# Optimization experiments

Measured on AMD Instinct MI355X. Metric: run time of the kernel, lower is better.

## Reference

```python
import jax, jax.numpy as jnp
import numpy as np

B, N, D_IN, D_OUT = 16, 2048, 128, 128

def setup_inputs() -> dict:
    key = jax.random.key(0)
    ks = jax.random.split(key, 8)
    x = jax.random.normal(ks[0], (B, N, D_IN), dtype=jnp.float32)
    adj = jax.random.randint(ks[1], (N, N), 0, 2).astype(jnp.float32)
    # Conv1d(kernel_size=1) weights, PyTorch default uniform init scale
    s_emb = 1.0 / np.sqrt(D_IN)
    W_emb = jax.random.uniform(ks[2], (D_OUT, D_IN), jnp.float32, -s_emb, s_emb)
    b_emb = jax.random.uniform(ks[3], (D_OUT,), jnp.float32, -s_emb, s_emb)
    s_qk = 1.0 / np.sqrt(D_OUT)
    w_q = jax.random.uniform(ks[4], (D_OUT,), jnp.float32, -s_qk, s_qk)
    b_q = jax.random.uniform(ks[5], (1,), jnp.float32, -s_qk, s_qk)
    w_k = jax.random.uniform(ks[6], (D_OUT,), jnp.float32, -s_qk, s_qk)
    b_k = jax.random.uniform(ks[7], (1,), jnp.float32, -s_qk, s_qk)
    return {"x": x, "adj": adj, "W_emb": W_emb, "b_emb": b_emb,
            "w_q": w_q, "b_q": b_q, "w_k": w_k, "b_k": b_k}

def reference(x, adj, W_emb, b_emb, w_q, b_q, w_k, b_k):
    # emb_conv: 1x1 conv over node dim == per-node linear  [B,N,D_out]
    seq_fts = jnp.einsum('bni,oi->bno', x, W_emb) + b_emb
    # q_conv / k_conv: project to scalar per node  [B,N]
    q = jnp.einsum('bnd,d->bn', seq_fts, w_q) + b_q  # f_1_t squeezed
    k = jnp.einsum('bnd,d->bn', seq_fts, w_k) + b_k  # f_2_t squeezed
    # f[b,i,j] = f_1_t[b,0,j] + f_2_t^T[b,i,0] = q[b,j] + k[b,i]
    f = k[:, :, None] + q[:, None, :]                 # [B,N,N]
    f = jax.nn.leaky_relu(adj[None, :, :] * f, negative_slope=0.01)
    coefs = jax.nn.softmax(f, axis=1)                 # softmax over dim=1 (rows)
    vals = jnp.einsum('bij,bjd->bid', coefs, seq_fts)  # [B,N,D_out]
    return vals
```

## Files before the change

kernel.cpp:

```cpp
#include <hip/hip_runtime.h>
#include <hip/hip_bf16.h>
#include <stdint.h>

#define B_ 16
#define N_ 2048
#define D_ 128

typedef __bf16 bf16_t;
typedef bf16_t bf16x8 __attribute__((ext_vector_type(8)));
typedef float f32x4 __attribute__((ext_vector_type(4)));

__global__ __launch_bounds__(256) void k_pack_adj(const float* __restrict__ adj,
                                                  unsigned int* __restrict__ bits) {
    int t = blockIdx.x * 256 + threadIdx.x;
    float v = adj[t];
    unsigned long long m = __ballot(v > 0.5f);
    if ((t & 63) == 0) {
        int i = t >> 11;
        int j = t & 2047;
        bits[i * 64 + (j >> 5)]     = (unsigned int)m;
        bits[i * 64 + (j >> 5) + 1] = (unsigned int)(m >> 32);
    }
}

__global__ __launch_bounds__(256, 1) void k_emb(const float* __restrict__ x,
                                                const float* __restrict__ W,
                                                const float* __restrict__ be,
                                                const float* __restrict__ wq,
                                                const float* __restrict__ wk,
                                                float* __restrict__ sfT,
                                                float* __restrict__ qa,
                                                float* __restrict__ ka) {
    __shared__ float xs[32][132];
    __shared__ float ws[32][132];
    __shared__ float qs[128], ks[128];
    int b  = blockIdx.y;
    int n0 = blockIdx.x * 128;
    int tid = threadIdx.x;
    int tx = tid & 15, ty = tid >> 4;
    if (tid < 128) { qs[tid] = 0.f; ks[tid] = 0.f; }

    float acc[8][8] = {};
    f32x4 xr[4], wr[4];

    auto loadregs = [&](int kc) {
#pragma unroll
        for (int s = 0; s < 4; ++s) {
            int p = tid + 256 * s;
            int n = p >> 3, kq = p & 7;
            xr[s] = *(const f32x4*)(x + ((size_t)(b * N_ + n0 + n)) * D_ + kc * 32 + kq * 4);
            wr[s] = *(const f32x4*)(W + (size_t)n * D_ + kc * 32 + kq * 4);
        }
    };
    auto writelds = [&]() {
#pragma unroll
        for (int s = 0; s < 4; ++s) {
            int p = tid + 256 * s;
            int n = p >> 3, kq = p & 7;
#pragma unroll
            for (int u = 0; u < 4; ++u) {
                xs[kq * 4 + u][n] = xr[s][u];
                ws[kq * 4 + u][n] = wr[s][u];
            }
        }
    };

    loadregs(0);
    for (int kc = 0; kc < 4; ++kc) {
        writelds();
        __syncthreads();
        if (kc < 3) loadregs(kc + 1);
        for (int k = 0; k < 32; ++k) {
            f32x4 xv0 = *(const f32x4*)&xs[k][tx * 8];
            f32x4 xv1 = *(const f32x4*)&xs[k][tx * 8 + 4];
            f32x4 wv0 = *(const f32x4*)&ws[k][ty * 8];
            f32x4 wv1 = *(const f32x4*)&ws[k][ty * 8 + 4];
#pragma unroll
            for (int i = 0; i < 8; ++i) {
                float xi = (i < 4) ? xv0[i] : xv1[i - 4];
#pragma unroll
                for (int j = 0; j < 8; ++j) {
                    float wj = (j < 4) ? wv0[j] : wv1[j - 4];
                    acc[i][j] += xi * wj;
                }
            }
        }
        __syncthreads();
    }

    float qp[8] = {}, kp[8] = {};
#pragma unroll
    for (int j = 0; j < 8; ++j) {
        int d = ty * 8 + j;
        float bj  = be[d];
        float wqj = wq[d];
        float wkj = wk[d];
        f32x4 o0, o1;
#pragma unroll
        for (int i = 0; i < 4; ++i) { o0[i] = acc[i][j] + bj; o1[i] = acc[4 + i][j] + bj; }
#pragma unroll
        for (int i = 0; i < 4; ++i) {
            qp[i]     += o0[i] * wqj;  kp[i]     += o0[i] * wkj;
            qp[4 + i] += o1[i] * wqj;  kp[4 + i] += o1[i] * wkj;
        }
        float* dst = sfT + ((size_t)b * D_ + d) * N_ + n0 + tx * 8;
        *(f32x4*)dst = o0;
        *(f32x4*)(dst + 4) = o1;
    }
#pragma unroll
    for (int i = 0; i < 8; ++i) {
        atomicAdd(&qs[tx * 8 + i], qp[i]);
        atomicAdd(&ks[tx * 8 + i], kp[i]);
    }
    __syncthreads();
    if (tid < 128) {
        qa[b * N_ + n0 + tid] = qs[tid];
        ka[b * N_ + n0 + tid] = ks[tid];
    }
}

__global__ __launch_bounds__(256) void k_exp(const float* __restrict__ bq,
                                             const float* __restrict__ bk,
                                             float* __restrict__ qa, float* __restrict__ ka,
                                             float* __restrict__ Eq, float* __restrict__ eqs,
                                             float* __restrict__ Ek, float* __restrict__ eks) {
    int t = blockIdx.x * 256 + threadIdx.x;
    float aq = qa[t] + bq[0];
    float ak = ka[t] + bk[0];
    qa[t] = aq;            ka[t] = ak;
    Eq[t] = expf(aq);      eqs[t] = expf(0.01f * aq);
    Ek[t] = expf(ak);      eks[t] = expf(0.01f * ak);
}

__global__ __launch_bounds__(256) void k_denom(const unsigned int* __restrict__ bits,
                                               const float* __restrict__ qa,
                                               const float* __restrict__ ka,
                                               const float* __restrict__ Eq,
                                               const float* __restrict__ eqs,
                                               const float* __restrict__ Ek,
                                               const float* __restrict__ eks,
                                               float* __restrict__ denom) {
    int jt  = blockIdx.x;
    int b   = blockIdx.y;
    int seg = blockIdx.z;
    int j = jt * 256 + threadIdx.x;
    float qj  = qa[b * N_ + j];
    float Eqj = Eq[b * N_ + j];
    float eqj = eqs[b * N_ + j];
    int shift = j & 31;
    int wid   = j >> 5;
    float acc = 0.f;
    int i0 = seg * 256;
#pragma unroll 8
    for (int i = i0; i < i0 + 256; ++i) {
        float kk  = ka[b * N_ + i];
        float Ekk = Ek[b * N_ + i];
        float ekk = eks[b * N_ + i];
        unsigned int w = bits[i * 64 + wid];
        float z  = kk + qj;
        float f1 = z > 0.f ? Ekk : ekk;
        float f2 = z > 0.f ? Eqj : eqj;
        float v  = f1 * f2;
        acc += ((w >> shift) & 1u) ? v : 1.0f;
    }
    atomicAdd(&denom[b * N_ + j], acc);
}

__global__ __launch_bounds__(256) void k_scale(const float* __restrict__ sfT,
                                               const float* __restrict__ denom,
                                               bf16_t* __restrict__ Pt) {
    size_t t = (size_t)blockIdx.x * 256 + threadIdx.x;
    int j  = (int)(t & (N_ - 1));
    int bd = (int)(t >> 11);
    int b  = bd >> 7;
    float v = sfT[t] / denom[b * N_ + j];
    Pt[t] = (bf16_t)v;
}

__global__ __launch_bounds__(256, 1) void k_attn(const float* __restrict__ qa,
                                                 const float* __restrict__ ka,
                                                 const float* __restrict__ Eq,
                                                 const float* __restrict__ eqs,
                                                 const float* __restrict__ Ek,
                                                 const float* __restrict__ eks,
                                                 const unsigned int* __restrict__ bits,
                                                 const bf16_t* __restrict__ Pt,
                                                 float* __restrict__ out) {
    __shared__ __align__(16) bf16_t lds[2][128 * 64];
    int b     = blockIdx.y;
    int ibase = blockIdx.x * 128;
    int tid   = threadIdx.x;
    int w     = tid >> 6;
    int lane  = tid & 63;
    int m16   = lane & 15;
    int quad  = lane >> 4;
    int i0    = ibase + w * 32;

    int iA = i0 + m16, iB = i0 + 16 + m16;
    float kR0  = ka[b * N_ + iA],  kR1  = ka[b * N_ + iB];
    float EkR0 = Ek[b * N_ + iA],  EkR1 = Ek[b * N_ + iB];
    float ekR0 = eks[b * N_ + iA], ekR1 = eks[b * N_ + iB];
    const unsigned int* br0 = bits + (size_t)iA * 64;
    const unsigned int* br1 = bits + (size_t)iB * 64;
    const float* qp  = qa  + b * N_;
    const float* Eqp = Eq  + b * N_;
    const float* eqp = eqs + b * N_;
    const bf16_t* PtB = Pt + (size_t)b * D_ * N_;

    f32x4 acc[2][8];
#pragma unroll
    for (int c = 0; c < 2; ++c)
#pragma unroll
        for (int nt = 0; nt < 8; ++nt) acc[c][nt] = (f32x4){0.f, 0.f, 0.f, 0.f};

    auto stage = [&](int bufi, int jb) {
#pragma unroll
        for (int t = 0; t < 4; ++t) {
            int off = (w * 4 + t) * 1024 + lane * 16;
            int d   = off >> 7;
            int g   = ((off & 127) >> 4) ^ (d & 7);
            const bf16_t* gp = PtB + (size_t)d * N_ + jb + g * 8;
            __builtin_amdgcn_global_load_lds(
                (const __attribute__((address_space(1))) void*)gp,
                (__attribute__((address_space(3))) void*)((char*)(&lds[bufi][0]) + (w * 4 + t) * 1024),
                16, 0, 0);
        }
    };

    stage(0, 0);
    __syncthreads();
    int buf = 0;
    for (int step = 0; step < N_ / 64; ++step) {
        int jb = step * 64;
        if (step + 1 < N_ / 64) stage(buf ^ 1, jb + 64);

        bf16x8 af[2][2];
#pragma unroll
        for (int h = 0; h < 2; ++h) {
            int j0 = jb + h * 32 + quad * 8;
            f32x4 q0 = *(const f32x4*)(qp + j0);
            f32x4 q1 = *(const f32x4*)(qp + j0 + 4);
            f32x4 E0 = *(const f32x4*)(Eqp + j0);
            f32x4 E1 = *(const f32x4*)(Eqp + j0 + 4);
            f32x4 e0 = *(const f32x4*)(eqp + j0);
            f32x4 e1 = *(const f32x4*)(eqp + j0 + 4);
            unsigned int w0 = br0[(jb >> 5) + h];
            unsigned int w1 = br1[(jb >> 5) + h];
#pragma unroll
            for (int t = 0; t < 8; ++t) {
                float qv = (t < 4) ? q0[t] : q1[t - 4];
                float Ev = (t < 4) ? E0[t] : E1[t - 4];
                float ev = (t < 4) ? e0[t] : e1[t - 4];
                int bit = quad * 8 + t;
                {
                    float z = kR0 + qv;
                    float v = ((z > 0.f) ? EkR0 : ekR0) * ((z > 0.f) ? Ev : ev);
                    af[0][h][t] = (bf16_t)(((w0 >> bit) & 1u) ? v : 1.0f);
                }
                {
                    float z = kR1 + qv;
                    float v = ((z > 0.f) ? EkR1 : ekR1) * ((z > 0.f) ? Ev : ev);
                    af[1][h][t] = (bf16_t)(((w1 >> bit) & 1u) ? v : 1.0f);
                }
            }
        }

#pragma unroll
        for (int h = 0; h < 2; ++h) {
            int cph = ((h * 4 + quad) ^ (m16 & 7)) * 8;
#pragma unroll
            for (int nt = 0; nt < 8; ++nt) {
                int d = nt * 16 + m16;
                bf16x8 bf = *(const bf16x8*)&lds[buf][d * 64 + cph];
                acc[0][nt] = __builtin_amdgcn_mfma_f32_16x16x32_bf16(af[0][h], bf, acc[0][nt], 0, 0, 0);
                acc[1][nt] = __builtin_amdgcn_mfma_f32_16x16x32_bf16(af[1][h], bf, acc[1][nt], 0, 0, 0);
            }
        }
        __syncthreads();
        buf ^= 1;
    }

#pragma unroll
    for (int c = 0; c < 2; ++c) {
        int irow = i0 + c * 16 + quad * 4;
#pragma unroll
        for (int nt = 0; nt < 8; ++nt) {
            int d = nt * 16 + m16;
#pragma unroll
            for (int r = 0; r < 4; ++r)
                out[((size_t)b * N_ + irow + r) * D_ + d] = acc[c][nt][r];
        }
    }
}

extern "C" void kernel_launch(void* const* d_in, const int* in_sizes, int n_in,
                              void* d_out, int out_size, void* d_ws, size_t ws_size,
                              hipStream_t stream) {
    const float* x   = (const float*)d_in[0];
    const float* adj = (const float*)d_in[1];
    const float* W   = (const float*)d_in[2];
    const float* be  = (const float*)d_in[3];
    const float* wq  = (const float*)d_in[4];
    const float* bq  = (const float*)d_in[5];
    const float* wk  = (const float*)d_in[6];
    const float* bk  = (const float*)d_in[7];
    float* out = (float*)d_out;

    char* ws = (char*)d_ws;
    size_t off = 0;
    float* sfT = (float*)(ws + off);  off += (size_t)B_ * D_ * N_ * 4;
    bf16_t* Pt = (bf16_t*)(ws + off); off += (size_t)B_ * D_ * N_ * 2;
    float* qa  = (float*)(ws + off);  off += (size_t)B_ * N_ * 4;
    float* ka  = (float*)(ws + off);  off += (size_t)B_ * N_ * 4;
    float* denom = (float*)(ws + off); off += (size_t)B_ * N_ * 4;
    float* Eq  = (float*)(ws + off);  off += (size_t)B_ * N_ * 4;
    float* eqs = (float*)(ws + off);  off += (size_t)B_ * N_ * 4;
    float* Ek  = (float*)(ws + off);  off += (size_t)B_ * N_ * 4;
    float* eks = (float*)(ws + off);  off += (size_t)B_ * N_ * 4;
    unsigned int* bits = (unsigned int*)(ws + off); off += (size_t)N_ * 64 * 4;

    hipMemsetAsync(denom, 0, (size_t)B_ * N_ * 4, stream);

    k_pack_adj<<<N_ * N_ / 256, 256, 0, stream>>>(adj, bits);
    k_emb<<<dim3(N_ / 128, B_), 256, 0, stream>>>(x, W, be, wq, wk, sfT, qa, ka);
    k_exp<<<B_ * N_ / 256, 256, 0, stream>>>(bq, bk, qa, ka, Eq, eqs, Ek, eks);
    k_denom<<<dim3(8, 16, 8), 256, 0, stream>>>(bits, qa, ka, Eq, eqs, Ek, eks, denom);
    k_scale<<<B_ * D_ * N_ / 256, 256, 0, stream>>>(sfT, denom, Pt);
    k_attn<<<dim3(N_ / 128, B_), 256, 0, stream>>>(qa, ka, Eq, eqs, Ek, eks, bits, Pt, out);
}
```

Baseline: 224.1 us.

## Fuse exp into embedding kernel, split attention D across 8 waves, vectorize scale

The embedding kernel now uses 64-node tiles at two blocks per CU, and it computes the exp terms directly, which removes the separate k_exp launch. The attention kernel now runs 512 threads, with each wave owning half of the output D columns. This halves accumulator registers per wave and doubles waves per block, though each wave now recomputes the attention coefficients. k_scale processes four elements per thread and uses a fast reciprocal. The k_denom unroll factor is raised.

Measured after the change: 216.1 us. 3.6% less time.

```diff
diff --git a/kernel.cpp b/kernel.cpp
--- a/kernel.cpp
+++ b/kernel.cpp
@@ -23,45 +23,57 @@
     }
 }
 
-__global__ __launch_bounds__(256, 1) void k_emb(const float* __restrict__ x,
+__global__ __launch_bounds__(256, 2) void k_emb(const float* __restrict__ x,
                                                 const float* __restrict__ W,
                                                 const float* __restrict__ be,
                                                 const float* __restrict__ wq,
+                                                const float* __restrict__ bq,
                                                 const float* __restrict__ wk,
+                                                const float* __restrict__ bk,
                                                 float* __restrict__ sfT,
-                                                float* __restrict__ qa,
-                                                float* __restrict__ ka) {
-    __shared__ float xs[32][132];
+                                                float* __restrict__ qa, float* __restrict__ ka,
+                                                float* __restrict__ Eq, float* __restrict__ eqs,
+                                                float* __restrict__ Ek, float* __restrict__ eks) {
+    __shared__ float xs[32][68];
     __shared__ float ws[32][132];
-    __shared__ float qs[128], ks[128];
+    __shared__ float qs[64], ks[64];
     int b  = blockIdx.y;
-    int n0 = blockIdx.x * 128;
+    int n0 = blockIdx.x * 64;
     int tid = threadIdx.x;
     int tx = tid & 15, ty = tid >> 4;
-    if (tid < 128) { qs[tid] = 0.f; ks[tid] = 0.f; }
-
-    float acc[8][8] = {};
-    f32x4 xr[4], wr[4];
+    if (tid < 64) { qs[tid] = 0.f; ks[tid] = 0.f; }
+
+    float acc[4][8] = {};
+    f32x4 xr[2], wr[4];
 
     auto loadregs = [&](int kc) {
 #pragma unroll
-        for (int s = 0; s < 4; ++s) {
+        for (int s = 0; s < 2; ++s) {
             int p = tid + 256 * s;
             int n = p >> 3, kq = p & 7;
             xr[s] = *(const f32x4*)(x + ((size_t)(b * N_ + n0 + n)) * D_ + kc * 32 + kq * 4);
-            wr[s] = *(const f32x4*)(W + (size_t)n * D_ + kc * 32 + kq * 4);
+        }
+#pragma unroll
+        for (int s = 0; s < 4; ++s) {
+            int p = tid + 256 * s;
+            int d = p >> 3, kq = p & 7;
+            wr[s] = *(const f32x4*)(W + (size_t)d * D_ + kc * 32 + kq * 4);
         }
     };
     auto writelds = [&]() {
 #pragma unroll
+        for (int s = 0; s < 2; ++s) {
+            int p = tid + 256 * s;
+            int n = p >> 3, kq = p & 7;
+#pragma unroll
+            for (int u = 0; u < 4; ++u) xs[kq * 4 + u][n] = xr[s][u];
+        }
+#pragma unroll
         for (int s = 0; s < 4; ++s) {
             int p = tid + 256 * s;
-            int n = p >> 3, kq = p & 7;
-#pragma unroll
-            for (int u = 0; u < 4; ++u) {
-                xs[kq * 4 + u][n] = xr[s][u];
-                ws[kq * 4 + u][n] = wr[s][u];
-            }
+            int d = p >> 3, kq = p & 7;
+#pragma unroll
+            for (int u = 0; u < 4; ++u) ws[kq * 4 + u][d] = wr[s][u];
         }
     };
 
@@ -70,66 +82,50 @@
         writelds();
         __syncthreads();
         if (kc < 3) loadregs(kc + 1);
+#pragma unroll 4
         for (int k = 0; k < 32; ++k) {
-            f32x4 xv0 = *(const f32x4*)&xs[k][tx * 8];
-            f32x4 xv1 = *(const f32x4*)&xs[k][tx * 8 + 4];
+            f32x4 xv  = *(const f32x4*)&xs[k][tx * 4];
             f32x4 wv0 = *(const f32x4*)&ws[k][ty * 8];
             f32x4 wv1 = *(const f32x4*)&ws[k][ty * 8 + 4];
 #pragma unroll
-            for (int i = 0; i < 8; ++i) {
-                float xi = (i < 4) ? xv0[i] : xv1[i - 4];
-#pragma unroll
-                for (int j = 0; j < 8; ++j) {
-                    float wj = (j < 4) ? wv0[j] : wv1[j - 4];
-                    acc[i][j] += xi * wj;
-                }
-            }
+            for (int i = 0; i < 4; ++i)
+#pragma unroll
+                for (int j = 0; j < 8; ++j)
+                    acc[i][j] += xv[i] * ((j < 4) ? wv0[j] : wv1[j - 4]);
         }
         __syncthreads();
     }
 
-    float qp[8] = {}, kp[8] = {};
+    float qp[4] = {}, kp[4] = {};
 #pragma unroll
     for (int j = 0; j < 8; ++j) {
         int d = ty * 8 + j;
         float bj  = be[d];
         float wqj = wq[d];
         float wkj = wk[d];
-        f32x4 o0, o1;
-#pragma unroll
-        for (int i = 0; i < 4; ++i) { o0[i] = acc[i][j] + bj; o1[i] = acc[4 + i][j] + bj; }
+        f32x4 o;
 #pragma unroll
         for (int i = 0; i < 4; ++i) {
-            qp[i]     += o0[i] * wqj;  kp[i]     += o0[i] * wkj;
-            qp[4 + i] += o1[i] * wqj;  kp[4 + i] += o1[i] * wkj;
-        }
-        float* dst = sfT + ((size_t)b * D_ + d) * N_ + n0 + tx * 8;
-        *(f32x4*)dst = o0;
-        *(f32x4*)(dst + 4) = o1;
-    }
-#pragma unroll
-    for (int i = 0; i < 8; ++i) {
-        atomicAdd(&qs[tx * 8 + i], qp[i]);
-        atomicAdd(&ks[tx * 8 + i], kp[i]);
+            o[i] = acc[i][j] + bj;
+            qp[i] += o[i] * wqj;
+            kp[i] += o[i] * wkj;
+        }
+        *(f32x4*)(sfT + ((size_t)b * D_ + d) * N_ + n0 + tx * 4) = o;
+    }
+#pragma unroll
+    for (int i = 0; i < 4; ++i) {
+        atomicAdd(&qs[tx * 4 + i], qp[i]);
+        atomicAdd(&ks[tx * 4 + i], kp[i]);
     }
     __syncthreads();
-    if (tid < 128) {
-        qa[b * N_ + n0 + tid] = qs[tid];
-        ka[b * N_ + n0 + tid] = ks[tid];
-    }
-}
-
-__global__ __launch_bounds__(256) void k_exp(const float* __restrict__ bq,
-                                             const float* __restrict__ bk,
-                                             float* __restrict__ qa, float* __restrict__ ka,
-                                             float* __restrict__ Eq, float* __restrict__ eqs,
-                                             float* __restrict__ Ek, float* __restrict__ eks) {
-    int t = blockIdx.x * 256 + threadIdx.x;
-    float aq = qa[t] + bq[0];
-    float ak = ka[t] + bk[0];
-    qa[t] = aq;            ka[t] = ak;
-    Eq[t] = expf(aq);      eqs[t] = expf(0.01f * aq);
-    Ek[t] = expf(ak);      eks[t] = expf(0.01f * ak);
+    if (tid < 64) {
+        int idx = b * N_ + n0 + tid;
+        float aq = qs[tid] + bq[0];
+        float ak = ks[tid] + bk[0];
+        qa[idx] = aq;          ka[idx] = ak;
+        Eq[idx] = expf(aq);    eqs[idx] = expf(0.01f * aq);
+        Ek[idx] = expf(ak);    eks[idx] = expf(0.01f * ak);
+    }
 }
 
 __global__ __launch_bounds__(256) void k_denom(const unsigned int* __restrict__ bits,
@@ -151,7 +147,7 @@
     int wid   = j >> 5;
     float acc = 0.f;
     int i0 = seg * 256;
-#pragma unroll 8
+#pragma unroll 16
     for (int i = i0; i < i0 + 256; ++i) {
         float kk  = ka[b * N_ + i];
         float Ekk = Ek[b * N_ + i];
@@ -169,15 +165,19 @@
 __global__ __launch_bounds__(256) void k_scale(const float* __restrict__ sfT,
                                                const float* __restrict__ denom,
                                                bf16_t* __restrict__ Pt) {
-    size_t t = (size_t)blockIdx.x * 256 + threadIdx.x;
-    int j  = (int)(t & (N_ - 1));
-    int bd = (int)(t >> 11);
-    int b  = bd >> 7;
-    float v = sfT[t] / denom[b * N_ + j];
-    Pt[t] = (bf16_t)v;
-}
-
-__global__ __launch_bounds__(256, 1) void k_attn(const float* __restrict__ qa,
+    size_t t4 = ((size_t)blockIdx.x * 256 + threadIdx.x) * 4;
+    int j  = (int)(t4 & (N_ - 1));
+    int b  = (int)(t4 >> 18);
+    f32x4 sv = *(const f32x4*)(sfT + t4);
+    f32x4 dv = *(const f32x4*)(denom + b * N_ + j);
+    bf16_t o[4];
+#pragma unroll
+    for (int u = 0; u < 4; ++u)
+        o[u] = (bf16_t)(sv[u] * __builtin_amdgcn_rcpf(dv[u]));
+    *(uint2*)(Pt + t4) = *(uint2*)o;
+}
+
+__global__ __launch_bounds__(512, 2) void k_attn(const float* __restrict__ qa,
                                                  const float* __restrict__ ka,
                                                  const float* __restrict__ Eq,
                                                  const float* __restrict__ eqs,
@@ -194,7 +194,9 @@
     int lane  = tid & 63;
     int m16   = lane & 15;
     int quad  = lane >> 4;
-    int i0    = ibase + w * 32;
+    int ig    = w & 3;
+    int d0    = (w >> 2) * 64;
+    int i0    = ibase + ig * 32;
 
     int iA = i0 + m16, iB = i0 + 16 + m16;
     float kR0  = ka[b * N_ + iA],  kR1  = ka[b * N_ + iB];
@@ -207,22 +209,22 @@
     const float* eqp = eqs + b * N_;
     const bf16_t* PtB = Pt + (size_t)b * D_ * N_;
 
-    f32x4 acc[2][8];
+    f32x4 acc[2][4];
 #pragma unroll
     for (int c = 0; c < 2; ++c)
 #pragma unroll
-        for (int nt = 0; nt < 8; ++nt) acc[c][nt] = (f32x4){0.f, 0.f, 0.f, 0.f};
+        for (int nt = 0; nt < 4; ++nt) acc[c][nt] = (f32x4){0.f, 0.f, 0.f, 0.f};
 
     auto stage = [&](int bufi, int jb) {
 #pragma unroll
-        for (int t = 0; t < 4; ++t) {
-            int off = (w * 4 + t) * 1024 + lane * 16;
+        for (int t = 0; t < 2; ++t) {
+            int off = (w * 2 + t) * 1024 + lane * 16;
             int d   = off >> 7;
             int g   = ((off & 127) >> 4) ^ (d & 7);
             const bf16_t* gp = PtB + (size_t)d * N_ + jb + g * 8;
             __builtin_amdgcn_global_load_lds(
                 (const __attribute__((address_space(1))) void*)gp,
-                (__attribute__((address_space(3))) void*)((char*)(&lds[bufi][0]) + (w * 4 + t) * 1024),
+                (__attribute__((address_space(3))) void*)((char*)(&lds[bufi][0]) + (w * 2 + t) * 1024),
                 16, 0, 0);
         }
     };
@@ -234,23 +236,30 @@
         int jb = step * 64;
         if (step + 1 < N_ / 64) stage(buf ^ 1, jb + 64);
 
-        bf16x8 af[2][2];
+        f32x4 q0[2], q1[2], E0[2], E1[2], e0[2], e1[2];
 #pragma unroll
         for (int h = 0; h < 2; ++h) {
             int j0 = jb + h * 32 + quad * 8;
-            f32x4 q0 = *(const f32x4*)(qp + j0);
-            f32x4 q1 = *(const f32x4*)(qp + j0 + 4);
-            f32x4 E0 = *(const f32x4*)(Eqp + j0);
-            f32x4 E1 = *(const f32x4*)(Eqp + j0 + 4);
-            f32x4 e0 = *(const f32x4*)(eqp + j0);
-            f32x4 e1 = *(const f32x4*)(eqp + j0 + 4);
-            unsigned int w0 = br0[(jb >> 5) + h];
-            unsigned int w1 = br1[(jb >> 5) + h];
+            q0[h] = *(const f32x4*)(qp  + j0);
+            q1[h] = *(const f32x4*)(qp  + j0 + 4);
+            E0[h] = *(const f32x4*)(Eqp + j0);
+            E1[h] = *(const f32x4*)(Eqp + j0 + 4);
+            e0[h] = *(const f32x4*)(eqp + j0);
+            e1[h] = *(const f32x4*)(eqp + j0 + 4);
+        }
+        uint2 wb0 = *(const uint2*)&br0[jb >> 5];
+        uint2 wb1 = *(const uint2*)&br1[jb >> 5];
+
+        bf16x8 af[2][2];
+#pragma unroll
+        for (int h = 0; h < 2; ++h) {
+            unsigned int w0 = h ? wb0.y : wb0.x;
+            unsigned int w1 = h ? wb1.y : wb1.x;
 #pragma unroll
             for (int t = 0; t < 8; ++t) {
-                float qv = (t < 4) ? q0[t] : q1[t - 4];
-                float Ev = (t < 4) ? E0[t] : E1[t - 4];
-                float ev = (t < 4) ? e0[t] : e1[t - 4];
+                float qv = (t < 4) ? q0[h][t] : q1[h][t - 4];
+                float Ev = (t < 4) ? E0[h][t] : E1[h][t - 4];
+                float ev = (t < 4) ? e0[h][t] : e1[h][t - 4];
                 int bit = quad * 8 + t;
                 {
                     float z = kR0 + qv;
@@ -269,8 +278,8 @@
         for (int h = 0; h < 2; ++h) {
             int cph = ((h * 4 + quad) ^ (m16 & 7)) * 8;
 #pragma unroll
-            for (int nt = 0; nt < 8; ++nt) {
-                int d = nt * 16 + m16;
+            for (int nt = 0; nt < 4; ++nt) {
+                int d = d0 + nt * 16 + m16;
                 bf16x8 bf = *(const bf16x8*)&lds[buf][d * 64 + cph];
                 acc[0][nt] = __builtin_amdgcn_mfma_f32_16x16x32_bf16(af[0][h], bf, acc[0][nt], 0, 0, 0);
                 acc[1][nt] = __builtin_amdgcn_mfma_f32_16x16x32_bf16(af[1][h], bf, acc[1][nt], 0, 0, 0);
@@ -284,8 +293,8 @@
     for (int c = 0; c < 2; ++c) {
         int irow = i0 + c * 16 + quad * 4;
 #pragma unroll
-        for (int nt = 0; nt < 8; ++nt) {
-            int d = nt * 16 + m16;
+        for (int nt = 0; nt < 4; ++nt) {
+            int d = d0 + nt * 16 + m16;
 #pragma unroll
             for (int r = 0; r < 4; ++r)
                 out[((size_t)b * N_ + irow + r) * D_ + d] = acc[c][nt][r];
@@ -322,9 +331,9 @@
     hipMemsetAsync(denom, 0, (size_t)B_ * N_ * 4, stream);
 
     k_pack_adj<<<N_ * N_ / 256, 256, 0, stream>>>(adj, bits);
-    k_emb<<<dim3(N_ / 128, B_), 256, 0, stream>>>(x, W, be, wq, wk, sfT, qa, ka);
-    k_exp<<<B_ * N_ / 256, 256, 0, stream>>>(bq, bk, qa, ka, Eq, eqs, Ek, eks);
+    k_emb<<<dim3(N_ / 64, B_), 256, 0, stream>>>(x, W, be, wq, bq, wk, bk,
+                                                 sfT, qa, ka, Eq, eqs, Ek, eks);
     k_denom<<<dim3(8, 16, 8), 256, 0, stream>>>(bits, qa, ka, Eq, eqs, Ek, eks, denom);
-    k_scale<<<B_ * D_ * N_ / 256, 256, 0, stream>>>(sfT, denom, Pt);
-    k_attn<<<dim3(N_ / 128, B_), 256, 0, stream>>>(qa, ka, Eq, eqs, Ek, eks, bits, Pt, out);
-}
+    k_scale<<<B_ * D_ * N_ / 1024, 256, 0, stream>>>(sfT, denom, Pt);
+    k_attn<<<dim3(N_ / 128, B_), 512, 0, stream>>>(qa, ka, Eq, eqs, Ek, eks, bits, Pt, out);
+}
```
